# Performance work log

Measured on AMD Instinct MI355X. Metric: run time of the kernel, lower is better.

Reference implementation:

```python
import jax, jax.numpy as jnp
import numpy as np
import math

HIDDEN = 2048
NUM_HEADS = 32
NUM_KV_HEADS = 8
HEAD_DIM = HIDDEN // NUM_HEADS
GROUPS = NUM_HEADS // NUM_KV_HEADS
B, S = 2, 2048


def setup_inputs() -> dict:
    key = jax.random.key(0)
    ks = jax.random.split(key, 9)
    sc = 1.0 / math.sqrt(HIDDEN)
    x = jax.random.normal(ks[0], (B, S, HIDDEN), dtype=jnp.float32)
    # causal mask: 1 where attention allowed, 0 where masked
    mask = jnp.tril(jnp.ones((S, S), dtype=jnp.int32))[None, None, :, :]
    Wq = jax.random.normal(ks[1], (HIDDEN, HIDDEN), dtype=jnp.float32) * sc
    bq = jnp.zeros((HIDDEN,), dtype=jnp.float32)
    Wk = jax.random.normal(ks[2], (NUM_KV_HEADS * HEAD_DIM, HIDDEN), dtype=jnp.float32) * sc
    bk = jnp.zeros((NUM_KV_HEADS * HEAD_DIM,), dtype=jnp.float32)
    Wv = jax.random.normal(ks[3], (NUM_KV_HEADS * HEAD_DIM, HIDDEN), dtype=jnp.float32) * sc
    bv = jnp.zeros((NUM_KV_HEADS * HEAD_DIM,), dtype=jnp.float32)
    Wo = jax.random.normal(ks[4], (HIDDEN, HIDDEN), dtype=jnp.float32) * sc
    bo = jnp.zeros((HIDDEN,), dtype=jnp.float32)
    return {"x": x, "mask": mask, "Wq": Wq, "bq": bq, "Wk": Wk, "bk": bk,
            "Wv": Wv, "bv": bv, "Wo": Wo, "bo": bo}


def reference(x, mask, Wq, bq, Wk, bk, Wv, bv, Wo, bo):
    b, s, _ = x.shape
    # projections (torch Linear: y = x @ W.T + b)
    Q = (x @ Wq.T + bq).reshape(b, s, NUM_HEADS, HEAD_DIM).transpose(0, 2, 1, 3)  # b h s d
    K = (x @ Wk.T + bk).reshape(b, s, NUM_KV_HEADS, HEAD_DIM).transpose(0, 2, 1, 3)
    V = (x @ Wv.T + bv).reshape(b, s, NUM_KV_HEADS, HEAD_DIM).transpose(0, 2, 1, 3)
    # repeat_kv expansion
    K = jnp.repeat(K, GROUPS, axis=1)  # b h s d
    V = jnp.repeat(V, GROUPS, axis=1)
    scores = jnp.einsum('bhqd,bhkd->bhqk', Q, K) / math.sqrt(HEAD_DIM)
    scores = jnp.where(mask == 0, jnp.float32(-jnp.inf), scores)
    w = jax.nn.softmax(scores, axis=-1)
    # dropout is identity in eval mode
    out = jnp.einsum('bhqk,bhkd->bhqd', w, V)
    out = out.transpose(0, 2, 1, 3).reshape(b, s, HIDDEN)
    return out @ Wo.T + bo
```

## Files before the change

kernel.cpp:

```cpp
#include <hip/hip_runtime.h>
#include <hip/hip_bf16.h>
#include <stdint.h>

#define HID   2048
#define SLEN  2048
#define NB    2
#define NHEADS 32
#define NKVH   8
#define HDIM   64
#define KVW    512

typedef __bf16 bf16_t;
typedef __bf16 bf16x2 __attribute__((ext_vector_type(2)));
typedef __bf16 bf16x4 __attribute__((ext_vector_type(4)));
typedef __bf16 bf16x8 __attribute__((ext_vector_type(8)));
typedef float  f32x4  __attribute__((ext_vector_type(4)));

__device__ __forceinline__ f32x4 mfma16(bf16x8 a, bf16x8 b, f32x4 c) {
  return __builtin_amdgcn_mfma_f32_16x16x32_bf16(a, b, c, 0, 0, 0);
}

__device__ __forceinline__ void gl2lds16(const bf16_t* g, bf16_t* l) {
  __builtin_amdgcn_global_load_lds(
      (const __attribute__((address_space(1))) void*)g,
      (__attribute__((address_space(3))) void*)l,
      16, 0, 0);
}

__device__ __forceinline__ float fast_exp2(float x) {
#if __has_builtin(__builtin_amdgcn_exp2f)
  return __builtin_amdgcn_exp2f(x);
#else
  return __expf(x * 0.69314718f);
#endif
}

__device__ __forceinline__ bf16x8 ld8(const bf16_t* p) {
  return *(const bf16x8*)p;
}
__device__ __forceinline__ bf16x8 ld8(const float* p) {
  f32x4 a = *(const f32x4*)p;
  f32x4 b = *(const f32x4*)(p + 4);
  bf16x8 r;
  r[0] = (bf16_t)a[0]; r[1] = (bf16_t)a[1]; r[2] = (bf16_t)a[2]; r[3] = (bf16_t)a[3];
  r[4] = (bf16_t)b[0]; r[5] = (bf16_t)b[1]; r[6] = (bf16_t)b[2]; r[7] = (bf16_t)b[3];
  return r;
}

__device__ __forceinline__ uint32_t pack2(float a, float b) {
  bf16x2 t; t[0] = (bf16_t)a; t[1] = (bf16_t)b;
  return __builtin_bit_cast(uint32_t, t);
}

__device__ __forceinline__ void st_c(bf16_t* p, float v) { *p = (bf16_t)v; }
__device__ __forceinline__ void st_c(float*  p, float v) { *p = v; }

__global__ __launch_bounds__(256) void cvt_kernel(
    const float* __restrict__ x,  const float* __restrict__ wq,
    const float* __restrict__ wk, const float* __restrict__ wv,
    const float* __restrict__ wo,
    const float* __restrict__ bq, const float* __restrict__ bk,
    const float* __restrict__ bv,
    bf16_t* xb, bf16_t* wqb, bf16_t* wkb, bf16_t* wvb, bf16_t* wob,
    float* bcat)
{
  if (blockIdx.y >= 5) {
    const float* fs; float* fd; size_t n;
    if (blockIdx.y == 5)      { fs = bq; fd = bcat;        n = HID; }
    else if (blockIdx.y == 6) { fs = bk; fd = bcat + HID;  n = KVW; }
    else                      { fs = bv; fd = bcat + HID + KVW; n = KVW; }
    const size_t stride4 = (size_t)gridDim.x * 256 * 4;
    for (size_t i = ((size_t)blockIdx.x * 256 + threadIdx.x) * 4; i < n; i += stride4)
      *(f32x4*)(fd + i) = *(const f32x4*)(fs + i);
    return;
  }
  const float* s; bf16_t* d; size_t n;
  switch (blockIdx.y) {
    case 0:  s = x;  d = xb;  n = (size_t)NB * SLEN * HID; break;
    case 1:  s = wq; d = wqb; n = (size_t)HID * HID; break;
    case 2:  s = wk; d = wkb; n = (size_t)KVW * HID; break;
    case 3:  s = wv; d = wvb; n = (size_t)KVW * HID; break;
    default: s = wo; d = wob; n = (size_t)HID * HID; break;
  }
  const size_t stride = (size_t)gridDim.x * 256 * 8;
  for (size_t i = ((size_t)blockIdx.x * 256 + threadIdx.x) * 8; i < n; i += stride)
    *(bf16x8*)(d + i) = ld8(s + i);
}

__device__ __forceinline__ bf16x8 ldfrag(const bf16_t* __restrict__ Lh, int r, int g) {
  return *(const bf16x8*)(Lh + r * 64 + ((g ^ (r & 7)) << 3));
}

template <int Q>
__device__ __forceinline__ void mfma_quad(const bf16x8 (&af)[2][2],
                                          const bf16x8 (&bfr)[4][2],
                                          f32x4 (&acc)[8][4]) {
#pragma unroll
  for (int ks = 0; ks < 2; ++ks)
#pragma unroll
    for (int i = 0; i < 2; ++i)
#pragma unroll
      for (int ni = 0; ni < 4; ++ni)
        acc[2 * Q + i][ni] = mfma16(af[i][ks], bfr[ni][ks], acc[2 * Q + i][ni]);
}

__device__ __forceinline__ void phase_barrier() {
  __builtin_amdgcn_s_barrier();
  asm volatile("" ::: "memory");
}

__device__ __forceinline__ void gemm256_core(
    const bf16_t* __restrict__ Ag,
    const bf16_t* __restrict__ Bg,
    bf16_t* __restrict__ lds, f32x4 (&acc)[8][4])
{
  const int tid  = threadIdx.x;
  const int lane = tid & 63;
  const int w    = tid >> 6;
  const int fr   = lane & 15;
  const int quad = lane >> 4;
  const int wr   = w >> 2;
  const int wc   = w & 3;
  const int rbB  = (wc & 1) * 64;

  bf16_t* A0 = lds;
  bf16_t* B0 = lds + 16384;
  bf16_t* A1 = lds + 32768;
  bf16_t* B1 = lds + 49152;
  const bf16_t* Ar0 = A0 + wr * 8192;
  const bf16_t* Br0 = B0 + (wc >> 1) * 8192;
  const bf16_t* Ar1 = A1 + wr * 8192;
  const bf16_t* Br1 = B1 + (wc >> 1) * 8192;

  const f32x4 z4 = {0.f, 0.f, 0.f, 0.f};
#pragma unroll
  for (int i = 0; i < 8; ++i)
#pragma unroll
    for (int j = 0; j < 4; ++j) acc[i][j] = z4;

  auto STAGE = [&](const bf16_t* __restrict__ Gp, bf16_t* __restrict__ Lh) {
#pragma unroll
    for (int j = 0; j < 2; ++j) {
      const int s = j * 512 + tid;
      const int r = s >> 3;
      const int g = (s & 7) ^ (r & 7);
      gl2lds16(Gp + (size_t)r * HID + g * 8, Lh + s * 8);
    }
  };

  STAGE(Bg,                  B0);
  STAGE(Bg + 128 * HID,      B0 + 8192);
  STAGE(Ag,                  A0);
  STAGE(Ag + 128 * HID,      A0 + 8192);
  STAGE(Bg + 64,             B1);
  STAGE(Bg + 128 * HID + 64, B1 + 8192);
  asm volatile("s_waitcnt vmcnt(4)" ::: "memory");
  phase_barrier();

  bf16x8 bfr[4][2], af[2][2];

#pragma unroll 1
  for (int it = 0; it < 16; ++it) {
    const bool more = (it < 15);
    const size_t k1 = (size_t)(2 * it + 1) * 64;
    const size_t k2 = (size_t)(2 * it + 2) * 64;
    const size_t k3 = (size_t)(2 * it + 3) * 64;

#pragma unroll
    for (int ni = 0; ni < 4; ++ni)
#pragma unroll
      for (int ks = 0; ks < 2; ++ks)
        bfr[ni][ks] = ldfrag(Br0, rbB + ni * 16 + fr, ks * 4 + quad);
#pragma unroll
    for (int i = 0; i < 2; ++i)
#pragma unroll
      for (int ks = 0; ks < 2; ++ks)
        af[i][ks] = ldfrag(Ar0, i * 16 + fr, ks * 4 + quad);
    STAGE(Ag + k1, A1);
    phase_barrier();
    asm volatile("s_waitcnt lgkmcnt(0)" ::: "memory");
    __builtin_amdgcn_s_setprio(1);
    mfma_quad<0>(af, bfr, acc);
    __builtin_amdgcn_s_setprio(0);
    phase_barrier();

#pragma unroll
    for (int i = 0; i < 2; ++i)
#pragma unroll
      for (int ks = 0; ks < 2; ++ks)
        af[i][ks] = ldfrag(Ar0, 32 + i * 16 + fr, ks * 4 + quad);
    STAGE(Ag + 128 * HID + k1, A1 + 8192);
    phase_barrier();
    asm volatile("s_waitcnt lgkmcnt(0)" ::: "memory");
    __builtin_amdgcn_s_setprio(1);
    mfma_quad<1>(af, bfr, acc);
    __builtin_amdgcn_s_setprio(0);
    phase_barrier();

#pragma unroll
    for (int i = 0; i < 2; ++i)
#pragma unroll
      for (int ks = 0; ks < 2; ++ks)
        af[i][ks] = ldfrag(Ar0, 64 + i * 16 + fr, ks * 4 + quad);
    if (more) STAGE(Bg + k2, B0);
    phase_barrier();
    asm volatile("s_waitcnt lgkmcnt(0)" ::: "memory");
    __builtin_amdgcn_s_setprio(1);
    mfma_quad<2>(af, bfr, acc);
    __builtin_amdgcn_s_setprio(0);
    phase_barrier();

#pragma unroll
    for (int i = 0; i < 2; ++i)
#pragma unroll
      for (int ks = 0; ks < 2; ++ks)
        af[i][ks] = ldfrag(Ar0, 96 + i * 16 + fr, ks * 4 + quad);
    if (more) STAGE(Bg + 128 * HID + k2, B0 + 8192);
    phase_barrier();
    asm volatile("s_waitcnt lgkmcnt(0)" ::: "memory");
    __builtin_amdgcn_s_setprio(1);
    mfma_quad<3>(af, bfr, acc);
    __builtin_amdgcn_s_setprio(0);
    if (more) { asm volatile("s_waitcnt vmcnt(4)" ::: "memory"); }
    else      { asm volatile("s_waitcnt vmcnt(0)" ::: "memory"); }
    phase_barrier();

#pragma unroll
    for (int ni = 0; ni < 4; ++ni)
#pragma unroll
      for (int ks = 0; ks < 2; ++ks)
        bfr[ni][ks] = ldfrag(Br1, rbB + ni * 16 + fr, ks * 4 + quad);
#pragma unroll
    for (int i = 0; i < 2; ++i)
#pragma unroll
      for (int ks = 0; ks < 2; ++ks)
        af[i][ks] = ldfrag(Ar1, i * 16 + fr, ks * 4 + quad);
    if (more) STAGE(Ag + k2, A0);
    phase_barrier();
    asm volatile("s_waitcnt lgkmcnt(0)" ::: "memory");
    __builtin_amdgcn_s_setprio(1);
    mfma_quad<0>(af, bfr, acc);
    __builtin_amdgcn_s_setprio(0);
    phase_barrier();

#pragma unroll
    for (int i = 0; i < 2; ++i)
#pragma unroll
      for (int ks = 0; ks < 2; ++ks)
        af[i][ks] = ldfrag(Ar1, 32 + i * 16 + fr, ks * 4 + quad);
    if (more) STAGE(Ag + 128 * HID + k2, A0 + 8192);
    phase_barrier();
    asm volatile("s_waitcnt lgkmcnt(0)" ::: "memory");
    __builtin_amdgcn_s_setprio(1);
    mfma_quad<1>(af, bfr, acc);
    __builtin_amdgcn_s_setprio(0);
    phase_barrier();

#pragma unroll
    for (int i = 0; i < 2; ++i)
#pragma unroll
      for (int ks = 0; ks < 2; ++ks)
        af[i][ks] = ldfrag(Ar1, 64 + i * 16 + fr, ks * 4 + quad);
    if (more) STAGE(Bg + k3, B1);
    phase_barrier();
    asm volatile("s_waitcnt lgkmcnt(0)" ::: "memory");
    __builtin_amdgcn_s_setprio(1);
    mfma_quad<2>(af, bfr, acc);
    __builtin_amdgcn_s_setprio(0);
    phase_barrier();

#pragma unroll
    for (int i = 0; i < 2; ++i)
#pragma unroll
      for (int ks = 0; ks < 2; ++ks)
        af[i][ks] = ldfrag(Ar1, 96 + i * 16 + fr, ks * 4 + quad);
    if (more) STAGE(Bg + 128 * HID + k3, B1 + 8192);
    phase_barrier();
    asm volatile("s_waitcnt lgkmcnt(0)" ::: "memory");
    __builtin_amdgcn_s_setprio(1);
    mfma_quad<3>(af, bfr, acc);
    __builtin_amdgcn_s_setprio(0);
    if (more) { asm volatile("s_waitcnt vmcnt(4)" ::: "memory"); }
    phase_barrier();
  }
}

__global__ __launch_bounds__(512, 2) void qkv8_kernel(
    const bf16_t* __restrict__ xb, const bf16_t* __restrict__ Wcat,
    const float* __restrict__ bcat,
    bf16_t* __restrict__ Qb, bf16_t* __restrict__ Kb, bf16_t* __restrict__ VbT)
{
  __shared__ __align__(16) bf16_t lds[65536];
  const int cb = blockIdx.x;
  const int mb = blockIdx.y;
  f32x4 acc[8][4];
  gemm256_core(xb + (size_t)mb * 256 * HID, Wcat + (size_t)cb * 256 * HID, lds, acc);

  const int tid = threadIdx.x, lane = tid & 63, w = tid >> 6;
  const int fr = lane & 15, quad = lane >> 4, wr = w >> 2, wc = w & 3;
#pragma unroll
  for (int ni = 0; ni < 4; ++ni) {
    const int gcol = cb * 256 + wc * 64 + ni * 16 + fr;
    const float bz = bcat[gcol];
#pragma unroll
    for (int mi = 0; mi < 8; ++mi) {
      const int grow = mb * 256 + wr * 128 + mi * 16 + quad * 4;
      if (cb < 8) {
#pragma unroll
        for (int r = 0; r < 4; ++r)
          Qb[(size_t)(grow + r) * HID + gcol] = (bf16_t)(acc[mi][ni][r] + bz);
      } else if (cb < 10) {
        const int kc = gcol - 2048;
#pragma unroll
        for (int r = 0; r < 4; ++r)
          Kb[(size_t)(grow + r) * KVW + kc] = (bf16_t)(acc[mi][ni][r] + bz);
      } else {
        const int vc = gcol - 2560;
        const int b = grow >> 11, s = grow & 2047;
        bf16x4 pk;
#pragma unroll
        for (int r = 0; r < 4; ++r) pk[r] = (bf16_t)(acc[mi][ni][r] + bz);
        *(bf16x4*)&VbT[((size_t)(b * NKVH + (vc >> 6)) * HDIM + (vc & 63)) * SLEN + s] = pk;
      }
    }
  }
}

__global__ __launch_bounds__(512, 2) void oproj8_kernel(
    const bf16_t* __restrict__ A, const bf16_t* __restrict__ Wob,
    const float* __restrict__ bo, float* __restrict__ out)
{
  __shared__ __align__(16) bf16_t lds[65536];
  const int cb = blockIdx.x;
  const int mb = blockIdx.y;
  f32x4 acc[8][4];
  gemm256_core(A + (size_t)mb * 256 * HID, Wob + (size_t)cb * 256 * HID, lds, acc);

  const int tid = threadIdx.x, lane = tid & 63, w = tid >> 6;
  const int fr = lane & 15, quad = lane >> 4, wr = w >> 2, wc = w & 3;
#pragma unroll
  for (int ni = 0; ni < 4; ++ni) {
    const int gcol = cb * 256 + wc * 64 + ni * 16 + fr;
    const float bz = bo[gcol];
#pragma unroll
    for (int mi = 0; mi < 8; ++mi) {
      const int grow = mb * 256 + wr * 128 + mi * 16 + quad * 4;
#pragma unroll
      for (int r = 0; r < 4; ++r)
        out[(size_t)(grow + r) * HID + gcol] = acc[mi][ni][r] + bz;
    }
  }
}

template <typename AT, typename CT>
__device__ __forceinline__ void gemm128_tile(
    const AT* __restrict__ Ap, int lda,
    const float* __restrict__ Wp, int ldw,
    const float* __restrict__ biasp,
    CT* __restrict__ Cp, int ldc,
    int K)
{
  __shared__ __align__(16) bf16_t Al[128 * 32];
  __shared__ __align__(16) bf16_t Bl[128 * 32];

  const int tid  = threadIdx.x;
  const int lane = tid & 63;
  const int w    = tid >> 6;
  const int fr   = lane & 15;
  const int quad = lane >> 4;
  const int wm   = (w >> 1) * 64;
  const int wn   = (w & 1) * 64;

  const f32x4 z4 = {0.f, 0.f, 0.f, 0.f};
  f32x4 acc[4][4];
  for (int i = 0; i < 4; ++i)
    for (int j = 0; j < 4; ++j) acc[i][j] = z4;

  const int c0    = w * 2;
  const int srow0 = lane >> 2;
  const int skc   = (lane & 3) * 8;

  for (int k0 = 0; k0 < K; k0 += 32) {
    bf16x8 av[2], bv[2];
    for (int t = 0; t < 2; ++t) {
      const int r = (c0 + t) * 16 + srow0;
      av[t] = ld8(Ap + (size_t)r * lda + k0 + skc);
      bv[t] = ld8(Wp + (size_t)r * ldw + k0 + skc);
    }
    for (int t = 0; t < 2; ++t) {
      const int c = c0 + t;
      *(bf16x8*)&Al[c * 512 + lane * 8] = av[t];
      *(bf16x8*)&Bl[c * 512 + lane * 8] = bv[t];
    }
    __syncthreads();
    bf16x8 af[4], bfr[4];
    for (int mi = 0; mi < 4; ++mi)
      af[mi] = *(const bf16x8*)&Al[(wm + mi * 16 + fr) * 32 + quad * 8];
    for (int ni = 0; ni < 4; ++ni)
      bfr[ni] = *(const bf16x8*)&Bl[(wn + ni * 16 + fr) * 32 + quad * 8];
    for (int mi = 0; mi < 4; ++mi)
      for (int ni = 0; ni < 4; ++ni)
        acc[mi][ni] = mfma16(af[mi], bfr[ni], acc[mi][ni]);
    __syncthreads();
  }

  for (int ni = 0; ni < 4; ++ni) {
    const int col = wn + ni * 16 + fr;
    const float bz = biasp[col];
    for (int mi = 0; mi < 4; ++mi) {
      const int r0 = wm + mi * 16 + quad * 4;
      for (int r = 0; r < 4; ++r)
        st_c(Cp + (size_t)(r0 + r) * ldc + col, acc[mi][ni][r] + bz);
    }
  }
}

__global__ __launch_bounds__(256) void qkv_kernel(
    const float* __restrict__ x,
    const float* __restrict__ Wq, const float* __restrict__ bq,
    const float* __restrict__ Wk, const float* __restrict__ bk,
    const float* __restrict__ Wv, const float* __restrict__ bv,
    bf16_t* Qb, bf16_t* Kb, bf16_t* Vb)
{
  const int nb = blockIdx.x;
  const int mb = blockIdx.y;
  const float* W; const float* bias; bf16_t* C; int ldc;
  if (nb < 16)      { W = Wq + (size_t)nb * 128 * HID;  bias = bq + nb * 128;
                      C = Qb + nb * 128; ldc = HID; }
  else if (nb < 20) { const int j = nb - 16;
                      W = Wk + (size_t)j * 128 * HID;   bias = bk + j * 128;
                      C = Kb + j * 128; ldc = KVW; }
  else              { const int j = nb - 20;
                      W = Wv + (size_t)j * 128 * HID;   bias = bv + j * 128;
                      C = Vb + j * 128; ldc = KVW; }
  gemm128_tile<float, bf16_t>(x + (size_t)mb * 128 * HID, HID, W, HID, bias,
                              C + (size_t)mb * 128 * ldc, ldc, HID);
}

__global__ __launch_bounds__(256) void oproj_kernel(
    const bf16_t* __restrict__ A, const float* __restrict__ Wo,
    const float* __restrict__ bo, float* out)
{
  const int nb = blockIdx.x, mb = blockIdx.y;
  gemm128_tile<bf16_t, float>(A + (size_t)mb * 128 * HID, HID,
                              Wo + (size_t)nb * 128 * HID, HID,
                              bo + nb * 128,
                              out + (size_t)mb * 128 * HID + nb * 128, HID, HID);
}

__global__ __launch_bounds__(256) void vtrans_kernel(
    const bf16_t* __restrict__ Vb, bf16_t* __restrict__ VbT)
{
  __shared__ bf16_t T[64][72];
  const int st = blockIdx.x, kvh = blockIdx.y, b = blockIdx.z;
  const int tid = threadIdx.x;
  {
    const int row = tid >> 2;
    const int c16 = (tid & 3) * 16;
    const bf16_t* src =
        Vb + ((size_t)b * SLEN + st * 64 + row) * KVW + kvh * HDIM + c16;
    *(bf16x8*)&T[row][c16]     = *(const bf16x8*)(src);
    *(bf16x8*)&T[row][c16 + 8] = *(const bf16x8*)(src + 8);
  }
  __syncthreads();
  {
    const int d  = tid >> 2;
    const int sc = (tid & 3) * 16;
    bf16_t tmp[16];
    for (int j = 0; j < 16; ++j) tmp[j] = T[sc + j][d];
    bf16_t* dst = VbT + ((size_t)(b * NKVH + kvh) * HDIM + d) * SLEN + st * 64 + sc;
    *(bf16x8*)dst       = *(bf16x8*)&tmp[0];
    *(bf16x8*)(dst + 8) = *(bf16x8*)&tmp[8];
  }
}

__global__ __launch_bounds__(512, 4) void attn_kernel(
    const bf16_t* Q, const bf16_t* __restrict__ Kg,
    const bf16_t* __restrict__ VT, bf16_t* O)
{
  const int bid = blockIdx.x;
  const int kvh = bid & 7;
  const int jb  = bid >> 3;
  const int b   = jb >> 5;
  const int rem = jb & 31;
  const int h   = kvh * 4 + (rem & 3);
  const int pid = rem >> 2;

  const int tid  = threadIdx.x;
  const int lane = tid & 63;
  const int w    = tid >> 6;
  const int fr   = lane & 15;
  const int quad = lane >> 4;

  __shared__ __align__(16) bf16_t lds[32768];

  const size_t qbase = (size_t)b * SLEN;
  const bf16_t* VTh = VT + (size_t)(b * NKVH + kvh) * HDIM * SLEN;

  const int sig = ((quad & 1) << 1) | ((quad >> 1) & 1);
  const int fsw = (fr >> 1) & 3;
  const bool oddq = (quad & 1);

  bf16x8 ones8;
  {
    const bf16_t o1 = (bf16_t)(fr == 0 ? 1.0f : 0.0f);
#pragma unroll
    for (int j2 = 0; j2 < 8; ++j2) ones8[j2] = o1;
  }

  auto STAGE_KV = [&](int kt, bf16_t* KL) {
    const size_t krow0 = qbase + (size_t)kt * 128;
    bf16_t* VtL = KL + 8192;
#pragma unroll
    for (int jj = 0; jj < 2; ++jj) {
      const int s  = jj * 512 + tid;
      const int ks = s >> 9, kr = (s >> 2) & 127, c8 = (s & 3) ^ ((kr >> 1) & 3);
      gl2lds16(&Kg[(krow0 + kr) * KVW + kvh * HDIM + ks * 32 + c8 * 8],
               &KL[s * 8]);
    }
#pragma unroll
    for (int jj = 0; jj < 2; ++jj) {
      const int idx = jj * 512 + tid;
      const int kb = idx >> 8, d = (idx >> 2) & 63, c8 = (idx & 3) ^ ((d >> 1) & 3);
      gl2lds16(&VTh[(size_t)d * SLEN + kt * 128 + kb * 32 + c8 * 8],
               &VtL[idx * 8]);
    }
  };

  for (int half = 0; half < 2; ++half) {
    const int qt = half ? (15 - pid) : pid;
    const int q0 = qt * 128;

    bf16x8 qf[2];
#pragma unroll
    for (int ks = 0; ks < 2; ++ks)
      qf[ks] = *(const bf16x8*)&Q[(qbase + q0 + w * 16 + fr) * HID
                                  + h * HDIM + ks * 32 + quad * 8];

    const f32x4 z4 = {0.f, 0.f, 0.f, 0.f};
    f32x4 o_acc[4];
    f32x4 o_l = z4;
#pragma unroll
    for (int di = 0; di < 4; ++di) o_acc[di] = z4;

    const int ktmax = qt;
    const int qloc  = w * 16 + fr;

    STAGE_KV(0, lds);
    asm volatile("s_waitcnt vmcnt(0)" ::: "memory");
    phase_barrier();

    int cur = 0;
    for (int kt = 0; kt <= ktmax; ++kt) {
      bf16_t* KL  = lds + cur * 16384;
      bf16_t* VtL = KL + 8192;
      if (kt < ktmax) STAGE_KV(kt + 1, lds + (cur ^ 1) * 16384);

      f32x4 s8[8];
#pragma unroll
      for (int ki = 0; ki < 8; ++ki) s8[ki] = z4;
      __builtin_amdgcn_s_setprio(1);
#pragma unroll
      for (int ks = 0; ks < 2; ++ks)
#pragma unroll
        for (int ki = 0; ki < 8; ++ki) {
          bf16x8 kf = *(const bf16x8*)&KL[ks * 4096 + (ki * 16 + fr) * 32
                                          + ((quad ^ fsw) << 3)];
          s8[ki] = mfma16(kf, qf[ks], s8[ki]);
        }
      __builtin_amdgcn_s_setprio(0);

      const float C2 = 0.18033688f;
      const bool diag = (kt == ktmax);

#pragma unroll
      for (int m = 0; m < 4; ++m) {
        float pe[8];
#pragma unroll
        for (int ki2 = 0; ki2 < 2; ++ki2) {
          const int ki = 2 * m + ki2;
#pragma unroll
          for (int r = 0; r < 4; ++r) {
            float p = fast_exp2(s8[ki][r] * C2);
            if (diag && (ki * 16 + quad * 4 + r > qloc)) p = 0.f;
            pe[ki2 * 4 + r] = p;
          }
        }
        uint32_t pw0 = pack2(pe[0], pe[1]);
        uint32_t pw1 = pack2(pe[2], pe[3]);
        uint32_t pw2 = pack2(pe[4], pe[5]);
        uint32_t pw3 = pack2(pe[6], pe[7]);
        uint32_t x0 = oddq ? pw0 : pw2;
        uint32_t x1 = oddq ? pw1 : pw3;
        uint32_t r0 = (uint32_t)__shfl_xor((int)x0, 16);
        uint32_t r1 = (uint32_t)__shfl_xor((int)x1, 16);
        union { uint32_t u[4]; bf16x8 v; } pb;
        pb.u[0] = oddq ? r0 : pw0;
        pb.u[1] = oddq ? r1 : pw1;
        pb.u[2] = oddq ? pw2 : r0;
        pb.u[3] = oddq ? pw3 : r1;

        __builtin_amdgcn_s_setprio(1);
        o_l = mfma16(pb.v, ones8, o_l);
#pragma unroll
        for (int di = 0; di < 4; ++di) {
          bf16x8 vf = *(const bf16x8*)&VtL[m * 2048 + (di * 16 + fr) * 32
                                           + ((sig ^ fsw) << 3)];
          o_acc[di] = mfma16(pb.v, vf, o_acc[di]);
        }
        __builtin_amdgcn_s_setprio(0);
      }

      asm volatile("s_waitcnt vmcnt(0)" ::: "memory");
      phase_barrier();
      cur ^= 1;
    }

    bf16_t* OB = lds;
#pragma unroll
    for (int r = 0; r < 4; ++r) {
      const float l  = __shfl(o_l[r], lane & 48);
      const float rl = 1.f / l;
      const int q = w * 16 + quad * 4 + r;
#pragma unroll
      for (int di = 0; di < 4; ++di)
        OB[q * 64 + di * 16 + fr] = (bf16_t)(o_acc[di][r] * rl);
    }
    asm volatile("s_waitcnt lgkmcnt(0)" ::: "memory");
    phase_barrier();
    {
      const int row = tid >> 2;
      const int seg = tid & 3;
      bf16x8 v0 = *(const bf16x8*)&OB[row * 64 + seg * 16];
      bf16x8 v1 = *(const bf16x8*)&OB[row * 64 + seg * 16 + 8];
      bf16_t* dst = &O[(qbase + q0 + row) * HID + h * HDIM + seg * 16];
      *(bf16x8*)dst       = v0;
      *(bf16x8*)(dst + 8) = v1;
    }
    phase_barrier();
  }
}

extern "C" void kernel_launch(void* const* d_in, const int* in_sizes, int n_in,
                              void* d_out, int out_size, void* d_ws, size_t ws_size,
                              hipStream_t stream) {
  const float* x  = (const float*)d_in[0];
  const float* Wq = (const float*)d_in[2];
  const float* bq = (const float*)d_in[3];
  const float* Wk = (const float*)d_in[4];
  const float* bk = (const float*)d_in[5];
  const float* Wv = (const float*)d_in[6];
  const float* bv = (const float*)d_in[7];
  const float* Wo = (const float*)d_in[8];
  const float* bo = (const float*)d_in[9];
  float* out = (float*)d_out;

  const size_t M = (size_t)NB * SLEN;
  dim3 blk(256, 1, 1);

  const size_t needA = (M * HID
                        + (size_t)HID * HID
                        + (size_t)KVW * HID
                        + (size_t)KVW * HID
                        + (size_t)HID * HID
                        + M * HID
                        + M * KVW
                        + M * KVW) * 2
                       + (size_t)(HID + 2 * KVW) * sizeof(float);
  if (ws_size >= needA) {
    bf16_t* xb  = (bf16_t*)d_ws;
    bf16_t* Wqb = xb  + M * HID;
    bf16_t* Wkb = Wqb + (size_t)HID * HID;
    bf16_t* Wvb = Wkb + (size_t)KVW * HID;
    bf16_t* Wob = Wvb + (size_t)KVW * HID;
    bf16_t* Qb  = Wob + (size_t)HID * HID;
    bf16_t* Kb  = Qb  + M * HID;
    bf16_t* VbT = Kb  + M * KVW;
    float*  bcat = (float*)(VbT + M * KVW);

    cvt_kernel<<<dim3(1024, 8, 1), blk, 0, stream>>>(
        x, Wq, Wk, Wv, Wo, bq, bk, bv, xb, Wqb, Wkb, Wvb, Wob, bcat);
    qkv8_kernel<<<dim3(12, 16, 1), dim3(512, 1, 1), 0, stream>>>(
        xb, Wqb, bcat, Qb, Kb, VbT);
    attn_kernel<<<dim3(512, 1, 1), dim3(512, 1, 1), 0, stream>>>(Qb, Kb, VbT, Qb);
    oproj8_kernel<<<dim3(8, 16, 1), dim3(512, 1, 1), 0, stream>>>(
        Qb, Wob, bo, out);
  } else {
    bf16_t* Qb  = (bf16_t*)d_ws;
    bf16_t* Kb  = Qb + M * HID;
    bf16_t* Vb  = Kb + M * KVW;
    bf16_t* VbT = Vb + M * KVW;

    qkv_kernel<<<dim3(24, 32, 1), blk, 0, stream>>>(x, Wq, bq, Wk, bk, Wv, bv, Qb, Kb, Vb);
    vtrans_kernel<<<dim3(32, 8, 2), blk, 0, stream>>>(Vb, VbT);
    attn_kernel<<<dim3(512, 1, 1), dim3(512, 1, 1), 0, stream>>>(Qb, Kb, VbT, Qb);
    oproj_kernel<<<dim3(16, 32, 1), blk, 0, stream>>>(Qb, Wo, bo, out);
  }
}
```

Measured before the change: 299.8 us.

## Retile QKV and O-proj GEMMs to fill all CUs, with XCD-aware mapping and LDS-staged epilogues

The 256x256 GEMM core becomes a template over the N-tile width. QKV now uses 256x192 tiles (16x16=256 blocks) and the output projection uses 256x128 tiles (256 blocks), so the grid matches the CU count on MI355X instead of launching 192 or 128 blocks. Block indices are remapped by XCD so that neighbouring tiles share L2. Epilogues stage results through LDS so global stores are coalesced, and the V transpose is done from LDS. In exchange, each block reuses its tiles less and runs an extra LDS pass and barriers in the epilogue.

Result: faster. 285.8 us (-4.7%).

```diff
diff --git a/kernel.cpp b/kernel.cpp
--- a/kernel.cpp
+++ b/kernel.cpp
@@ -91,16 +91,24 @@
   return *(const bf16x8*)(Lh + r * 64 + ((g ^ (r & 7)) << 3));
 }
 
-template <int Q>
-__device__ __forceinline__ void mfma_quad(const bf16x8 (&af)[2][2],
-                                          const bf16x8 (&bfr)[4][2],
-                                          f32x4 (&acc)[8][4]) {
+template <int N>
+__device__ __forceinline__ void vm_wait() {
+  if constexpr (N == 0)      asm volatile("s_waitcnt vmcnt(0)" ::: "memory");
+  else if constexpr (N == 2) asm volatile("s_waitcnt vmcnt(2)" ::: "memory");
+  else if constexpr (N == 3) asm volatile("s_waitcnt vmcnt(3)" ::: "memory");
+  else                       asm volatile("s_waitcnt vmcnt(4)" ::: "memory");
+}
+
+template <int Q, int U>
+__device__ __forceinline__ void mfma_quadU(const bf16x8 (&af)[2][2],
+                                           const bf16x8 (&bfr)[U][2],
+                                           f32x4 (&acc)[8][U]) {
 #pragma unroll
   for (int ks = 0; ks < 2; ++ks)
 #pragma unroll
     for (int i = 0; i < 2; ++i)
 #pragma unroll
-      for (int ni = 0; ni < 4; ++ni)
+      for (int ni = 0; ni < U; ++ni)
         acc[2 * Q + i][ni] = mfma16(af[i][ks], bfr[ni][ks], acc[2 * Q + i][ni]);
 }
 
@@ -109,10 +117,11 @@
   asm volatile("" ::: "memory");
 }
 
-__device__ __forceinline__ void gemm256_core(
+template <int U>
+__device__ __forceinline__ void gemm_core_u(
     const bf16_t* __restrict__ Ag,
     const bf16_t* __restrict__ Bg,
-    bf16_t* __restrict__ lds, f32x4 (&acc)[8][4])
+    bf16_t* __restrict__ lds, f32x4 (&acc)[8][U])
 {
   const int tid  = threadIdx.x;
   const int lane = tid & 63;
@@ -121,43 +130,48 @@
   const int quad = lane >> 4;
   const int wr   = w >> 2;
   const int wc   = w & 3;
-  const int rbB  = (wc & 1) * 64;
 
   bf16_t* A0 = lds;
   bf16_t* B0 = lds + 16384;
-  bf16_t* A1 = lds + 32768;
-  bf16_t* B1 = lds + 49152;
-  const bf16_t* Ar0 = A0 + wr * 8192;
-  const bf16_t* Br0 = B0 + (wc >> 1) * 8192;
-  const bf16_t* Ar1 = A1 + wr * 8192;
-  const bf16_t* Br1 = B1 + (wc >> 1) * 8192;
+  bf16_t* A1 = B0 + U * 4096;
+  bf16_t* B1 = A1 + 16384;
 
   const f32x4 z4 = {0.f, 0.f, 0.f, 0.f};
 #pragma unroll
   for (int i = 0; i < 8; ++i)
 #pragma unroll
-    for (int j = 0; j < 4; ++j) acc[i][j] = z4;
-
-  auto STAGE = [&](const bf16_t* __restrict__ Gp, bf16_t* __restrict__ Lh) {
-#pragma unroll
-    for (int j = 0; j < 2; ++j) {
-      const int s = j * 512 + tid;
-      const int r = s >> 3;
-      const int g = (s & 7) ^ (r & 7);
-      gl2lds16(Gp + (size_t)r * HID + g * 8, Lh + s * 8);
-    }
+    for (int j = 0; j < U; ++j) acc[i][j] = z4;
+
+  auto STAGEU = [&](const bf16_t* __restrict__ Gp, bf16_t* __restrict__ Lb, int u) {
+    const int r = tid >> 3;
+    const int g = (tid & 7) ^ (r & 7);
+    gl2lds16(Gp + (size_t)(u * 64 + r) * HID + g * 8, Lb + u * 4096 + tid * 8);
   };
-
-  STAGE(Bg,                  B0);
-  STAGE(Bg + 128 * HID,      B0 + 8192);
-  STAGE(Ag,                  A0);
-  STAGE(Ag + 128 * HID,      A0 + 8192);
-  STAGE(Bg + 64,             B1);
-  STAGE(Bg + 128 * HID + 64, B1 + 8192);
-  asm volatile("s_waitcnt vmcnt(4)" ::: "memory");
+  auto LDB = [&](const bf16_t* __restrict__ Bb, bf16x8 (&bfr)[U][2]) {
+#pragma unroll
+    for (int ni = 0; ni < U; ++ni)
+#pragma unroll
+      for (int ks = 0; ks < 2; ++ks)
+        bfr[ni][ks] = ldfrag(Bb, wc * (16 * U) + ni * 16 + fr, ks * 4 + quad);
+  };
+  auto LDA = [&](const bf16_t* __restrict__ Ab, int q, bf16x8 (&af)[2][2]) {
+#pragma unroll
+    for (int i = 0; i < 2; ++i)
+#pragma unroll
+      for (int ks = 0; ks < 2; ++ks)
+        af[i][ks] = ldfrag(Ab, wr * 128 + q * 32 + i * 16 + fr, ks * 4 + quad);
+  };
+
+#pragma unroll
+  for (int u = 0; u < U; ++u) STAGEU(Bg, B0, u);
+#pragma unroll
+  for (int u = 0; u < 4; ++u) STAGEU(Ag, A0, u);
+#pragma unroll
+  for (int u = 0; u < U; ++u) STAGEU(Bg + 64, B1, u);
+  vm_wait<U>();
   phase_barrier();
 
-  bf16x8 bfr[4][2], af[2][2];
+  bf16x8 bfr[U][2], af[2][2];
 
 #pragma unroll 1
   for (int it = 0; it < 16; ++it) {
@@ -166,123 +180,100 @@
     const size_t k2 = (size_t)(2 * it + 2) * 64;
     const size_t k3 = (size_t)(2 * it + 3) * 64;
 
-#pragma unroll
-    for (int ni = 0; ni < 4; ++ni)
-#pragma unroll
-      for (int ks = 0; ks < 2; ++ks)
-        bfr[ni][ks] = ldfrag(Br0, rbB + ni * 16 + fr, ks * 4 + quad);
-#pragma unroll
-    for (int i = 0; i < 2; ++i)
-#pragma unroll
-      for (int ks = 0; ks < 2; ++ks)
-        af[i][ks] = ldfrag(Ar0, i * 16 + fr, ks * 4 + quad);
-    STAGE(Ag + k1, A1);
+    LDB(B0, bfr);
+    LDA(A0, 0, af);
+    STAGEU(Ag + k1, A1, 0); STAGEU(Ag + k1, A1, 1);
     phase_barrier();
     asm volatile("s_waitcnt lgkmcnt(0)" ::: "memory");
     __builtin_amdgcn_s_setprio(1);
-    mfma_quad<0>(af, bfr, acc);
+    mfma_quadU<0>(af, bfr, acc);
     __builtin_amdgcn_s_setprio(0);
     phase_barrier();
 
-#pragma unroll
-    for (int i = 0; i < 2; ++i)
-#pragma unroll
-      for (int ks = 0; ks < 2; ++ks)
-        af[i][ks] = ldfrag(Ar0, 32 + i * 16 + fr, ks * 4 + quad);
-    STAGE(Ag + 128 * HID + k1, A1 + 8192);
+    LDA(A0, 1, af);
+    STAGEU(Ag + k1, A1, 2); STAGEU(Ag + k1, A1, 3);
     phase_barrier();
     asm volatile("s_waitcnt lgkmcnt(0)" ::: "memory");
     __builtin_amdgcn_s_setprio(1);
-    mfma_quad<1>(af, bfr, acc);
+    mfma_quadU<1>(af, bfr, acc);
     __builtin_amdgcn_s_setprio(0);
     phase_barrier();
 
-#pragma unroll
-    for (int i = 0; i < 2; ++i)
-#pragma unroll
-      for (int ks = 0; ks < 2; ++ks)
-        af[i][ks] = ldfrag(Ar0, 64 + i * 16 + fr, ks * 4 + quad);
-    if (more) STAGE(Bg + k2, B0);
+    LDA(A0, 2, af);
+    if (more) {
+#pragma unroll
+      for (int u = 0; u < (U + 1) / 2; ++u) STAGEU(Bg + k2, B0, u);
+    }
     phase_barrier();
     asm volatile("s_waitcnt lgkmcnt(0)" ::: "memory");
     __builtin_amdgcn_s_setprio(1);
-    mfma_quad<2>(af, bfr, acc);
+    mfma_quadU<2>(af, bfr, acc);
     __builtin_amdgcn_s_setprio(0);
     phase_barrier();
 
-#pragma unroll
-    for (int i = 0; i < 2; ++i)
-#pragma unroll
-      for (int ks = 0; ks < 2; ++ks)
-        af[i][ks] = ldfrag(Ar0, 96 + i * 16 + fr, ks * 4 + quad);
-    if (more) STAGE(Bg + 128 * HID + k2, B0 + 8192);
+    LDA(A0, 3, af);
+    if (more) {
+#pragma unroll
+      for (int u = (U + 1) / 2; u < U; ++u) STAGEU(Bg + k2, B0, u);
+    }
     phase_barrier();
     asm volatile("s_waitcnt lgkmcnt(0)" ::: "memory");
     __builtin_amdgcn_s_setprio(1);
-    mfma_quad<3>(af, bfr, acc);
+    mfma_quadU<3>(af, bfr, acc);
     __builtin_amdgcn_s_setprio(0);
-    if (more) { asm volatile("s_waitcnt vmcnt(4)" ::: "memory"); }
-    else      { asm volatile("s_waitcnt vmcnt(0)" ::: "memory"); }
-    phase_barrier();
-
-#pragma unroll
-    for (int ni = 0; ni < 4; ++ni)
-#pragma unroll
-      for (int ks = 0; ks < 2; ++ks)
-        bfr[ni][ks] = ldfrag(Br1, rbB + ni * 16 + fr, ks * 4 + quad);
-#pragma unroll
-    for (int i = 0; i < 2; ++i)
-#pragma unroll
-      for (int ks = 0; ks < 2; ++ks)
-        af[i][ks] = ldfrag(Ar1, i * 16 + fr, ks * 4 + quad);
-    if (more) STAGE(Ag + k2, A0);
+    if (more) vm_wait<U>(); else vm_wait<0>();
+    phase_barrier();
+
+    LDB(B1, bfr);
+    LDA(A1, 0, af);
+    if (more) { STAGEU(Ag + k2, A0, 0); STAGEU(Ag + k2, A0, 1); }
     phase_barrier();
     asm volatile("s_waitcnt lgkmcnt(0)" ::: "memory");
     __builtin_amdgcn_s_setprio(1);
-    mfma_quad<0>(af, bfr, acc);
+    mfma_quadU<0>(af, bfr, acc);
     __builtin_amdgcn_s_setprio(0);
     phase_barrier();
 
-#pragma unroll
-    for (int i = 0; i < 2; ++i)
-#pragma unroll
-      for (int ks = 0; ks < 2; ++ks)
-        af[i][ks] = ldfrag(Ar1, 32 + i * 16 + fr, ks * 4 + quad);
-    if (more) STAGE(Ag + 128 * HID + k2, A0 + 8192);
+    LDA(A1, 1, af);
+    if (more) { STAGEU(Ag + k2, A0, 2); STAGEU(Ag + k2, A0, 3); }
     phase_barrier();
     asm volatile("s_waitcnt lgkmcnt(0)" ::: "memory");
     __builtin_amdgcn_s_setprio(1);
-    mfma_quad<1>(af, bfr, acc);
+    mfma_quadU<1>(af, bfr, acc);
     __builtin_amdgcn_s_setprio(0);
     phase_barrier();
 
-#pragma unroll
-    for (int i = 0; i < 2; ++i)
-#pragma unroll
-      for (int ks = 0; ks < 2; ++ks)
-        af[i][ks] = ldfrag(Ar1, 64 + i * 16 + fr, ks * 4 + quad);
-    if (more) STAGE(Bg + k3, B1);
+    LDA(A1, 2, af);
+    if (more) {
+#pragma unroll
+      for (int u = 0; u < (U + 1) / 2; ++u) STAGEU(Bg + k3, B1, u);
+    }
     phase_barrier();
     asm volatile("s_waitcnt lgkmcnt(0)" ::: "memory");
     __builtin_amdgcn_s_setprio(1);
-    mfma_quad<2>(af, bfr, acc);
+    mfma_quadU<2>(af, bfr, acc);
     __builtin_amdgcn_s_setprio(0);
     phase_barrier();
 
-#pragma unroll
-    for (int i = 0; i < 2; ++i)
-#pragma unroll
-      for (int ks = 0; ks < 2; ++ks)
-        af[i][ks] = ldfrag(Ar1, 96 + i * 16 + fr, ks * 4 + quad);
-    if (more) STAGE(Bg + 128 * HID + k3, B1 + 8192);
+    LDA(A1, 3, af);
+    if (more) {
+#pragma unroll
+      for (int u = (U + 1) / 2; u < U; ++u) STAGEU(Bg + k3, B1, u);
+    }
     phase_barrier();
     asm volatile("s_waitcnt lgkmcnt(0)" ::: "memory");
     __builtin_amdgcn_s_setprio(1);
-    mfma_quad<3>(af, bfr, acc);
+    mfma_quadU<3>(af, bfr, acc);
     __builtin_amdgcn_s_setprio(0);
-    if (more) { asm volatile("s_waitcnt vmcnt(4)" ::: "memory"); }
-    phase_barrier();
-  }
+    if (more) vm_wait<U>();
+    phase_barrier();
+  }
+}
+
+__device__ __forceinline__ void grid_map16(int orig, int& cb, int& mb) {
+  const int xcd = orig & 7, wp = orig >> 3;
+  cb = (xcd & 1) * 8 + (wp & 7);
+  mb = (xcd >> 1) * 4 + (wp >> 3);
 }
 
 __global__ __launch_bounds__(512, 2) void qkv8_kernel(
@@ -290,37 +281,62 @@
     const float* __restrict__ bcat,
     bf16_t* __restrict__ Qb, bf16_t* __restrict__ Kb, bf16_t* __restrict__ VbT)
 {
-  __shared__ __align__(16) bf16_t lds[65536];
-  const int cb = blockIdx.x;
-  const int mb = blockIdx.y;
-  f32x4 acc[8][4];
-  gemm256_core(xb + (size_t)mb * 256 * HID, Wcat + (size_t)cb * 256 * HID, lds, acc);
+  __shared__ __align__(16) bf16_t lds[57344];
+  int cb, mb;
+  grid_map16(blockIdx.x, cb, mb);
+
+  f32x4 acc[8][3];
+  gemm_core_u<3>(xb + (size_t)mb * 256 * HID, Wcat + (size_t)cb * 192 * HID,
+                 lds, acc);
 
   const int tid = threadIdx.x, lane = tid & 63, w = tid >> 6;
   const int fr = lane & 15, quad = lane >> 4, wr = w >> 2, wc = w & 3;
-#pragma unroll
-  for (int ni = 0; ni < 4; ++ni) {
-    const int gcol = cb * 256 + wc * 64 + ni * 16 + fr;
-    const float bz = bcat[gcol];
-#pragma unroll
-    for (int mi = 0; mi < 8; ++mi) {
-      const int grow = mb * 256 + wr * 128 + mi * 16 + quad * 4;
-      if (cb < 8) {
-#pragma unroll
-        for (int r = 0; r < 4; ++r)
-          Qb[(size_t)(grow + r) * HID + gcol] = (bf16_t)(acc[mi][ni][r] + bz);
-      } else if (cb < 10) {
-        const int kc = gcol - 2048;
-#pragma unroll
-        for (int r = 0; r < 4; ++r)
-          Kb[(size_t)(grow + r) * KVW + kc] = (bf16_t)(acc[mi][ni][r] + bz);
-      } else {
-        const int vc = gcol - 2560;
-        const int b = grow >> 11, s = grow & 2047;
-        bf16x4 pk;
-#pragma unroll
-        for (int r = 0; r < 4; ++r) pk[r] = (bf16_t)(acc[mi][ni][r] + bz);
-        *(bf16x4*)&VbT[((size_t)(b * NKVH + (vc >> 6)) * HDIM + (vc & 63)) * SLEN + s] = pk;
+  const int CP = 200;
+  bf16_t* C = lds;
+#pragma unroll
+  for (int ni = 0; ni < 3; ++ni) {
+    const int col = wc * 48 + ni * 16 + fr;
+    const float bz = bcat[cb * 192 + col];
+#pragma unroll
+    for (int mi = 0; mi < 8; ++mi)
+#pragma unroll
+      for (int r = 0; r < 4; ++r)
+        C[(wr * 128 + mi * 16 + quad * 4 + r) * CP + col] =
+            (bf16_t)(acc[mi][ni][r] + bz);
+  }
+  asm volatile("s_waitcnt lgkmcnt(0)" ::: "memory");
+  phase_barrier();
+
+#pragma unroll
+  for (int i = 0; i < 12; ++i) {
+    const unsigned task = (unsigned)(i * 512 + tid);
+    const unsigned row = task / 24u;
+    const unsigned cg  = task - row * 24u;
+    const int gcol0 = cb * 192 + (int)cg * 8;
+    const int grow  = mb * 256 + (int)row;
+    bf16x8 v = *(const bf16x8*)&C[row * CP + cg * 8];
+    if (gcol0 < 2048)
+      *(bf16x8*)&Qb[(size_t)grow * HID + gcol0] = v;
+    else if (gcol0 < 2560)
+      *(bf16x8*)&Kb[(size_t)grow * KVW + (gcol0 - 2048)] = v;
+  }
+  if (cb >= 13) {
+    const int colbase = (cb == 13) ? 64 : 0;
+    const int Nv = 192 - colbase;
+    const int b = mb >> 3;
+    const int s0 = (mb & 7) * 256;
+#pragma unroll
+    for (int i = 0; i < 12; ++i) {
+      const int task = i * 512 + tid;
+      const int vi = task >> 5, si = task & 31;
+      if (vi < Nv) {
+        const int col = colbase + vi;
+        const int vc  = cb * 192 + col - 2560;
+        bf16x8 pk;
+#pragma unroll
+        for (int j = 0; j < 8; ++j) pk[j] = C[(si * 8 + j) * CP + col];
+        *(bf16x8*)&VbT[((size_t)(b * NKVH + (vc >> 6)) * HDIM + (vc & 63)) * SLEN
+                       + s0 + si * 8] = pk;
       }
     }
   }
@@ -330,25 +346,42 @@
     const bf16_t* __restrict__ A, const bf16_t* __restrict__ Wob,
     const float* __restrict__ bo, float* __restrict__ out)
 {
-  __shared__ __align__(16) bf16_t lds[65536];
-  const int cb = blockIdx.x;
-  const int mb = blockIdx.y;
-  f32x4 acc[8][4];
-  gemm256_core(A + (size_t)mb * 256 * HID, Wob + (size_t)cb * 256 * HID, lds, acc);
+  __shared__ __align__(16) bf16_t lds[49152];
+  int cb, mb;
+  grid_map16(blockIdx.x, cb, mb);
+
+  f32x4 acc[8][2];
+  gemm_core_u<2>(A + (size_t)mb * 256 * HID, Wob + (size_t)cb * 128 * HID,
+                 lds, acc);
 
   const int tid = threadIdx.x, lane = tid & 63, w = tid >> 6;
   const int fr = lane & 15, quad = lane >> 4, wr = w >> 2, wc = w & 3;
-#pragma unroll
-  for (int ni = 0; ni < 4; ++ni) {
-    const int gcol = cb * 256 + wc * 64 + ni * 16 + fr;
-    const float bz = bo[gcol];
-#pragma unroll
-    for (int mi = 0; mi < 8; ++mi) {
-      const int grow = mb * 256 + wr * 128 + mi * 16 + quad * 4;
-#pragma unroll
-      for (int r = 0; r < 4; ++r)
-        out[(size_t)(grow + r) * HID + gcol] = acc[mi][ni][r] + bz;
-    }
+  const int CPF = 132;
+  float* Cf = (float*)lds;
+#pragma unroll
+  for (int s = 0; s < 2; ++s) {
+    if (wr == s) {
+#pragma unroll
+      for (int ni = 0; ni < 2; ++ni) {
+        const int col = wc * 32 + ni * 16 + fr;
+        const float bz = bo[cb * 128 + col];
+#pragma unroll
+        for (int mi = 0; mi < 8; ++mi)
+#pragma unroll
+          for (int r = 0; r < 4; ++r)
+            Cf[(mi * 16 + quad * 4 + r) * CPF + col] = acc[mi][ni][r] + bz;
+      }
+    }
+    asm volatile("s_waitcnt lgkmcnt(0)" ::: "memory");
+    phase_barrier();
+#pragma unroll
+    for (int i = 0; i < 8; ++i) {
+      const int task = i * 512 + tid;
+      const int row = task >> 5, cg = task & 31;
+      f32x4 v = *(const f32x4*)&Cf[row * CPF + cg * 4];
+      *(f32x4*)&out[(size_t)(mb * 256 + s * 128 + row) * HID + cb * 128 + cg * 4] = v;
+    }
+    phase_barrier();
   }
 }
 
@@ -680,10 +713,10 @@
 
     cvt_kernel<<<dim3(1024, 8, 1), blk, 0, stream>>>(
         x, Wq, Wk, Wv, Wo, bq, bk, bv, xb, Wqb, Wkb, Wvb, Wob, bcat);
-    qkv8_kernel<<<dim3(12, 16, 1), dim3(512, 1, 1), 0, stream>>>(
+    qkv8_kernel<<<dim3(256, 1, 1), dim3(512, 1, 1), 0, stream>>>(
         xb, Wqb, bcat, Qb, Kb, VbT);
     attn_kernel<<<dim3(512, 1, 1), dim3(512, 1, 1), 0, stream>>>(Qb, Kb, VbT, Qb);
-    oproj8_kernel<<<dim3(8, 16, 1), dim3(512, 1, 1), 0, stream>>>(
+    oproj8_kernel<<<dim3(256, 1, 1), dim3(512, 1, 1), 0, stream>>>(
         Qb, Wob, bo, out);
   } else {
     bf16_t* Qb  = (bf16_t*)d_ws;
```
